# Optimization experiments

Hardware: AMD Instinct MI355X
Metric: run time of the kernel (lower is better)

The kernel has to match this reference:

```python
import jax, jax.numpy as jnp
import numpy as np
from jax import lax

EPS = 1e-6
DN = ('NCHW', 'OIHW', 'NCHW')


def cconv2d(x, wr, wi, br, bi, padding, dilation, groups):
    """Complex conv2d: x [B,2,C,H,W]; (a+ib)*(c+id) convolution with per-part bias.
    real = conv(xr,wr)+br - (conv(xi,wi)+bi); imag = conv(xi,wr)+br + conv(xr,wi)+bi."""
    B = x.shape[0]
    x2 = jnp.concatenate([x[:, 0], x[:, 1]], axis=0)  # [2B,C,H,W] stack re/im in batch
    pad = [(padding[0], padding[0]), (padding[1], padding[1])]

    def conv(w):
        return lax.conv_general_dilated(x2, w, (1, 1), pad, rhs_dilation=dilation,
                                        dimension_numbers=DN, feature_group_count=groups)

    cr = conv(wr)
    ci = conv(wi)
    real = cr[:B] - ci[B:] + (br - bi)[None, :, None, None]
    imag = cr[B:] + ci[:B] + (br + bi)[None, :, None, None]
    return jnp.stack([real, imag], axis=1)


def parallel_conv1d(t, wr, wi, br, bi, ch_out, kernel, dilation=1):
    """Grouped per-frequency complex conv. t: [B,2,Cin,N,T] -> [B,2,ch_out,N,T] (causal)."""
    B, _, Cin, N, T = t.shape
    pad = kernel * dilation - dilation
    x = jnp.transpose(t, (0, 1, 3, 2, 4))  # [B,2,N,Cin,T]; channels=N, groups=N
    y = cconv2d(x, wr, wi, br, bi, (0, pad), (1, dilation), N)  # [B,2,N*ch_out,1,T+pad]
    y = y[..., pad:]  # trim -> causal, length T
    y = y.reshape(B, 2, N, ch_out, T)
    return jnp.transpose(y, (0, 1, 3, 2, 4))


def cAct(t):
    return jnp.stack([jnp.tanh(t[:, 0]), jax.nn.relu(t[:, 1])], axis=1)


def cLog(t):
    re, im = t[:, 0], t[:, 1]
    mag = jnp.sqrt(re * re + im * im)
    return jnp.stack([jnp.log(mag + EPS), jnp.arctan2(im, re)], axis=1)


def cExp(t):
    mag = jnp.exp(t[:, 0])
    return jnp.stack([mag * jnp.cos(t[:, 1]), mag * jnp.sin(t[:, 1])], axis=1)


FREQS, CH_IN, CH_INNER, FREQ_K, TIME_K, DIL = 256, 8, 32, 3, 5, 2


def setup_inputs() -> dict:
    key = jax.random.key(0)
    ks = jax.random.split(key, 17)
    s = 0.05
    d = {'tensor': jax.random.normal(ks[0], (4, 2, CH_IN, FREQS, 1000), jnp.float32)}
    # channel_shuffle: ParallelConv1d(freqs, ch_in, ch_inner, 1) -> weight [N*ch_inner,1,ch_in,1]
    d['cs_wr'] = jax.random.normal(ks[1], (FREQS * CH_INNER, 1, CH_IN, 1), jnp.float32) * s
    d['cs_wi'] = jax.random.normal(ks[2], (FREQS * CH_INNER, 1, CH_IN, 1), jnp.float32) * s
    d['cs_br'] = jax.random.normal(ks[3], (FREQS * CH_INNER,), jnp.float32) * s
    d['cs_bi'] = jax.random.normal(ks[4], (FREQS * CH_INNER,), jnp.float32) * s
    # freq_conv: depthwise ComplexConv2d(ch_inner, ch_inner, (freq_kernel,1), groups=ch_inner)
    d['fc_wr'] = jax.random.normal(ks[5], (CH_INNER, 1, FREQ_K, 1), jnp.float32) * s
    d['fc_wi'] = jax.random.normal(ks[6], (CH_INNER, 1, FREQ_K, 1), jnp.float32) * s
    d['fc_br'] = jax.random.normal(ks[7], (CH_INNER,), jnp.float32) * s
    d['fc_bi'] = jax.random.normal(ks[8], (CH_INNER,), jnp.float32) * s
    # time_conv: ParallelConv1d(freqs, ch_inner, ch_in, time_kernel, dilation)
    d['tc_wr'] = jax.random.normal(ks[9], (FREQS * CH_IN, 1, CH_INNER, TIME_K), jnp.float32) * s
    d['tc_wi'] = jax.random.normal(ks[10], (FREQS * CH_IN, 1, CH_INNER, TIME_K), jnp.float32) * s
    d['tc_br'] = jax.random.normal(ks[11], (FREQS * CH_IN,), jnp.float32) * s
    d['tc_bi'] = jax.random.normal(ks[12], (FREQS * CH_IN,), jnp.float32) * s
    # last: ParallelConv1d(freqs, ch_in, ch_in, 1)
    d['last_wr'] = jax.random.normal(ks[13], (FREQS * CH_IN, 1, CH_IN, 1), jnp.float32) * s
    d['last_wi'] = jax.random.normal(ks[14], (FREQS * CH_IN, 1, CH_IN, 1), jnp.float32) * s
    d['last_br'] = jax.random.normal(ks[15], (FREQS * CH_IN,), jnp.float32) * s
    d['last_bi'] = jax.random.normal(ks[16], (FREQS * CH_IN,), jnp.float32) * s
    return d


def reference(tensor, cs_wr, cs_wi, cs_br, cs_bi, fc_wr, fc_wi, fc_br, fc_bi,
              tc_wr, tc_wi, tc_br, tc_bi, last_wr, last_wi, last_br, last_bi):
    t = cLog(tensor)                                                    # [B,2,Cin,N,T]
    t = parallel_conv1d(t, cs_wr, cs_wi, cs_br, cs_bi, CH_INNER, 1)     # [B,2,Cinner,N,T]
    t = cAct(t)
    t = cconv2d(t, fc_wr, fc_wi, fc_br, fc_bi, (FREQ_K // 2, 0), (1, 1), CH_INNER)
    t = cAct(t)
    t = parallel_conv1d(t, tc_wr, tc_wi, tc_br, tc_bi, CH_IN, TIME_K, DIL)
    t = cAct(t)
    t = cExp(t)
    t = parallel_conv1d(t, last_wr, last_wi, last_br, last_bi, CH_IN, 1)
    return t
```

## Files before the change

### kernel.cpp

```cpp
#include <hip/hip_runtime.h>
#include <math.h>

#define TLEN 1000
#define NF 256
#define CIN 8
#define CMID 32
#define TK 5
#define TT 120
#define THA 128
#define T2R 136
#define SLS 72

#define CSW_OFF  0u
#define CB_OFF   1048576u
#define FCP_OFF  1114112u
#define FCB_OFF  1114880u
#define TCW_OFF  1115136u
#define TCB_OFF  3736576u
#define LA_OFF   3752960u
#define LAB_OFF  4015104u
#define XLOG_OFF 4031488u
#define WS_NEED  36799488u

typedef _Float16 f16x8 __attribute__((ext_vector_type(8)));
typedef _Float16 f16x4 __attribute__((ext_vector_type(4)));
typedef _Float16 f16x2 __attribute__((ext_vector_type(2)));
typedef float f32x4 __attribute__((ext_vector_type(4)));

__device__ __forceinline__ float ftanh(float x) {
    float e = __expf(2.0f * x);
    return 1.0f - 2.0f / (e + 1.0f);
}

__device__ __forceinline__ float fatan2(float y, float x) {
    float ax = fabsf(x), ay = fabsf(y);
    float mx = fmaxf(fmaxf(ax, ay), 1e-30f);
    float mn = fminf(ax, ay);
    float a = mn * __builtin_amdgcn_rcpf(mx);
    float s = a * a;
    float r = fmaf(s, fmaf(s, fmaf(s, fmaf(s, fmaf(s, -0.0117212f, 0.05265332f),
                -0.11643287f), 0.19354346f), -0.33262347f), 0.99997726f);
    r *= a;
    if (ay > ax) r = 1.5707964f - r;
    if (x < 0.0f) r = 3.1415927f - r;
    return copysignf(r, y);
}

__global__ __launch_bounds__(256) void mb_pack(
    const float* __restrict__ cswr, const float* __restrict__ cswi,
    const float* __restrict__ csbr, const float* __restrict__ csbi,
    const float* __restrict__ fcwr, const float* __restrict__ fcwi,
    const float* __restrict__ fcbr, const float* __restrict__ fcbi,
    const float* __restrict__ tcwr, const float* __restrict__ tcwi,
    const float* __restrict__ tcbr, const float* __restrict__ tcbi,
    const float* __restrict__ lawr, const float* __restrict__ lawi,
    const float* __restrict__ labr, const float* __restrict__ labi,
    unsigned char* __restrict__ ws)
{
    int e = blockIdx.x * 256 + threadIdx.x;
    if (e < 32768) {
        int fp = e >> 7, ca = (e >> 2) & 31, g = e & 3;
        f16x8 aRe = (f16x8){0,0,0,0,0,0,0,0}, aIm = (f16x8){0,0,0,0,0,0,0,0};
        if (g < 2) {
            const float* wr = cswr + ((size_t)fp*CMID + ca)*CIN + g*4;
            const float* wi = cswi + ((size_t)fp*CMID + ca)*CIN + g*4;
#pragma unroll
            for (int r = 0; r < 4; ++r) {
                float a = wr[r], bb = wi[r];
                aRe[2*r] = (_Float16)a;  aRe[2*r+1] = (_Float16)(-bb);
                aIm[2*r] = (_Float16)bb; aIm[2*r+1] = (_Float16)a;
            }
        }
        *(f16x8*)(ws + CSW_OFF + (size_t)e*32)      = aRe;
        *(f16x8*)(ws + CSW_OFF + (size_t)e*32 + 16) = aIm;
        return;
    }
    e -= 32768;
    if (e < 8192) {
        int fp = e >> 5, c = e & 31;
        float br = csbr[fp*CMID + c], bi = csbi[fp*CMID + c];
        *(float2*)(ws + CB_OFF + (size_t)e*8) = make_float2(br - bi, br + bi);
        return;
    }
    e -= 8192;
    if (e < 96) {
        int j = e / 32, c = e % 32;
        *(float2*)(ws + FCP_OFF + (size_t)e*8) = make_float2(fcwr[c*3 + j], fcwi[c*3 + j]);
        return;
    }
    e -= 96;
    if (e < 32) {
        *(float2*)(ws + FCB_OFF + (size_t)e*8) = make_float2(fcbr[e] - fcbi[e], fcbr[e] + fcbi[e]);
        return;
    }
    e -= 32;
    if (e < 163840) {
        int idx = e % 640;
        int f   = e / 640;
        int m   = idx / 40;
        int r2  = idx % 40;
        int g   = r2 / 10;
        int i10 = r2 % 10;
        int kt = i10 >> 1, kc = i10 & 1;
        int co = m & 7;
        f16x8 v;
#pragma unroll
        for (int j = 0; j < 8; ++j) {
            int ci = kc*16 + g*4 + (j >> 1);
            int p  = j & 1;
            float a  = tcwr[(((size_t)f*CIN + co)*CMID + ci)*TK + kt];
            float bb = tcwi[(((size_t)f*CIN + co)*CMID + ci)*TK + kt];
            float val = (m < 8) ? (p ? -bb : a) : (p ? a : bb);
            v[j] = (_Float16)val;
        }
        *(f16x8*)(ws + TCW_OFF + (size_t)e*16) = v;
        return;
    }
    e -= 163840;
    if (e < 4096) {
        int f = e >> 4, m = e & 15, co = m & 7;
        float br = tcbr[f*CIN + co], bi = tcbi[f*CIN + co];
        *(float*)(ws + TCB_OFF + (size_t)e*4) = (m >= 8) ? (br + bi) : (br - bi);
        return;
    }
    e -= 4096;
    if (e < 16384) {
        int f = e >> 6, m = (e >> 2) & 15, g = e & 3, co = m & 7;
        f16x8 v = (f16x8){0,0,0,0,0,0,0,0};
        if (g < 2) {
#pragma unroll
            for (int j = 0; j < 8; ++j) {
                int ci = g*4 + (j >> 1);
                int p  = j & 1;
                float a  = lawr[((size_t)f*CIN + co)*CIN + ci];
                float bb = lawi[((size_t)f*CIN + co)*CIN + ci];
                float val = (m < 8) ? (p ? -bb : a) : (p ? a : bb);
                v[j] = (_Float16)val;
            }
        }
        *(f16x8*)(ws + LA_OFF + (size_t)e*16) = v;
        return;
    }
    e -= 16384;
    if (e < 4096) {
        int f = e >> 4, m = e & 15, co = m & 7;
        float br = labr[f*CIN + co], bi = labi[f*CIN + co];
        *(float*)(ws + LAB_OFF + (size_t)e*4) = (m >= 8) ? (br + bi) : (br - bi);
    }
}

__global__ __launch_bounds__(256) void mb_xlog(
    const float* __restrict__ x, unsigned char* __restrict__ ws)
{
    const int tid = threadIdx.x;
    const int chunk = blockIdx.x;
    const int f = blockIdx.y;
    const int b = blockIdx.z;
    const int t00 = chunk * 128;

    __shared__ __align__(16) _Float16 sl[128 * 16];

    const float* xr_base = x + ((size_t)(b*2+0)*CIN)*NF*TLEN + (size_t)f*TLEN;
    const float* xi_base = x + ((size_t)(b*2+1)*CIN)*NF*TLEN + (size_t)f*TLEN;
#pragma unroll
    for (int it = 0; it < 4; ++it) {
        int i  = it*256 + tid;
        int tl = i & 127, ci = i >> 7;
        int tg = t00 + tl;
        float lr = 0.f, li = 0.f;
        if (tg < TLEN) {
            float vr = xr_base[(size_t)ci*NF*TLEN + tg];
            float vi = xi_base[(size_t)ci*NF*TLEN + tg];
            lr = __logf(sqrtf(fmaf(vr, vr, vi*vi)) + 1e-6f);
            li = fatan2(vi, vr);
        }
        *(f16x2*)&sl[tl*16 + ci*2] = (f16x2){(_Float16)lr, (_Float16)li};
    }
    __syncthreads();
    if (tid < 128) {
        int tg = t00 + tid;
        if (tg < TLEN) {
            unsigned char* dst = ws + XLOG_OFF + ((size_t)(b*NF + f)*1000 + tg)*32;
            *(f16x8*)dst        = *(const f16x8*)&sl[tid*16];
            *(f16x8*)(dst + 16) = *(const f16x8*)&sl[tid*16 + 8];
        }
    }
}

__device__ __forceinline__ int t2r_off(int tl, int kc, int g) {
    int byte = tl * 128 + kc * 64 + g * 16;
    byte ^= (tl & 7) << 4;
    return byte;
}

__global__ __launch_bounds__(256, 4) void mb_main(
    const unsigned char* __restrict__ ws, float* __restrict__ out)
{
    const int tid  = threadIdx.x;
    const int tb   = blockIdx.x;
    const int f    = blockIdx.y;
    const int b    = blockIdx.z;
    const int t0   = tb * TT;
    const int lane = tid & 63;
    const int w    = tid >> 6;
    const int col  = lane & 15;
    const int g    = lane >> 4;

    __shared__ __align__(16) unsigned char s_t2h[T2R * 128];
    __shared__ __align__(16) float s_y[THA][17];
    _Float16* s_e = (_Float16*)s_t2h;

    ((unsigned int*)s_t2h)[THA*32 + tid] = 0u;

    const f16x8*  cswp = (const f16x8*)(ws + CSW_OFF);
    const float4* cb4  = (const float4*)(ws + CB_OFF);
    const f16x8*  tcp  = (const f16x8*)(ws + TCW_OFF);
    const float4* tb4  = (const float4*)(ws + TCB_OFF);
    const f16x8*  lap  = (const f16x8*)(ws + LA_OFF);
    const float4* lb4  = (const float4*)(ws + LAB_OFF);

    const int cBase  = (w & 1) * 16;
    const int ntBase = (w >> 1) * 4;
    const int ca = cBase + col;
    const int cg = cBase + 4*g;

    int toff[4];
    {
        int tbv = t0 + ntBase*16 + col;
#pragma unroll
        for (int q = 0; q < 4; ++q) {
            int t = tbv + q*16; if (t > 999) t = 999;
            toff[q] = t*32 + (g & 1)*16;
        }
    }
    const int awoff = (ca*4 + g)*2;
    const int cboff = cg >> 1;

    f32x4 accR[4], accI[4];
#pragma unroll
    for (int q = 0; q < 4; ++q) { accR[q] = (f32x4){0,0,0,0}; accI[q] = (f32x4){0,0,0,0}; }

#define STAGE_A_J(J)                                                          \
    { const int fp = f - 1 + (J);                                             \
      if (fp >= 0 && fp < NF) {                                               \
        f16x8 aRe = cswp[fp*256 + awoff];                                     \
        f16x8 aIm = cswp[fp*256 + awoff + 1];                                 \
        float4 c01 = cb4[fp*16 + cboff], c23 = cb4[fp*16 + cboff + 1];        \
        float4 fc01 = *(const float4*)(ws + FCP_OFF + ((J)*32 + cg)*8);       \
        float4 fc23 = *(const float4*)(ws + FCP_OFF + ((J)*32 + cg)*8 + 16);  \
        const unsigned char* xb = ws + XLOG_OFF + (size_t)(b*NF + fp)*32000;  \
        float bm[4] = {c01.x, c01.z, c23.x, c23.z};                           \
        float bp[4] = {c01.y, c01.w, c23.y, c23.w};                           \
        float fr[4] = {fc01.x, fc01.z, fc23.x, fc23.z};                       \
        float fi[4] = {fc01.y, fc01.w, fc23.y, fc23.w};                       \
        _Pragma("unroll")                                                     \
        for (int q = 0; q < 4; ++q) {                                         \
            f16x8 bf = *(const f16x8*)(xb + toff[q]);                         \
            f32x4 dRe = __builtin_amdgcn_mfma_f32_16x16x32_f16(aRe, bf, (f32x4){0,0,0,0}, 0, 0, 0); \
            f32x4 dIm = __builtin_amdgcn_mfma_f32_16x16x32_f16(aIm, bf, (f32x4){0,0,0,0}, 0, 0, 0); \
            _Pragma("unroll")                                                 \
            for (int r = 0; r < 4; ++r) {                                     \
                float ar = ftanh(dRe[r] + bm[r]);                             \
                float ai = fmaxf(dIm[r] + bp[r], 0.f);                        \
                accR[q][r] = fmaf(fr[r], ar, fmaf(-fi[r], ai, accR[q][r]));   \
                accI[q][r] = fmaf(fr[r], ai, fmaf( fi[r], ar, accI[q][r]));   \
            }                                                                 \
        } } }

    STAGE_A_J(0)
    STAGE_A_J(1)
    STAGE_A_J(2)
#undef STAGE_A_J

    {
        float4 fb01 = *(const float4*)(ws + FCB_OFF + cg*8);
        float4 fb23 = *(const float4*)(ws + FCB_OFF + cg*8 + 16);
        float fbm[4] = {fb01.x, fb01.z, fb23.x, fb23.z};
        float fbp[4] = {fb01.y, fb01.w, fb23.y, fb23.w};
#pragma unroll
        for (int q = 0; q < 4; ++q) {
            int tp = ntBase*16 + q*16 + col;
            bool pad = (t0 + tp >= TLEN);
            f16x8 v;
#pragma unroll
            for (int r = 0; r < 4; ++r) {
                float tr = ftanh(accR[q][r] + fbm[r]);
                float ti = fmaxf(accI[q][r] + fbp[r], 0.f);
                v[2*r]   = (_Float16)tr;
                v[2*r+1] = (_Float16)ti;
            }
            if (pad) v = (f16x8){0,0,0,0,0,0,0,0};
            int addr = (tp*128 + cg*4) ^ ((tp & 7) << 4);
            *(f16x8*)&s_t2h[addr] = v;
        }
    }

    f16x8 afr[10];
    {
        int base = ((f*16 + col)*4 + g)*10;
#pragma unroll
        for (int kk = 0; kk < 10; ++kk) afr[kk] = tcp[base + kk];
    }
    __syncthreads();

    {
        const int tb0 = w * 32, tb1 = tb0 + 16;
        f32x4 acc0 = {0,0,0,0}, acc1 = {0,0,0,0};
#pragma unroll
        for (int kt = 0; kt < 5; ++kt) {
#pragma unroll
            for (int kc = 0; kc < 2; ++kc) {
                f16x8 b0 = *(const f16x8*)&s_t2h[t2r_off(tb0 + col + 2*kt, kc, g)];
                f16x8 b1 = *(const f16x8*)&s_t2h[t2r_off(tb1 + col + 2*kt, kc, g)];
                acc0 = __builtin_amdgcn_mfma_f32_16x16x32_f16(afr[kt*2+kc], b0, acc0, 0, 0, 0);
                acc1 = __builtin_amdgcn_mfma_f32_16x16x32_f16(afr[kt*2+kc], b1, acc1, 0, 0, 0);
            }
        }
        float4 tcb = tb4[f*4 + g];
        float tcbv[4] = {tcb.x, tcb.y, tcb.z, tcb.w};
#pragma unroll
        for (int r = 0; r < 4; ++r) {
            int mm = g*4 + r;
            s_y[tb0 + col][mm] = acc0[r] + tcbv[r];
            s_y[tb1 + col][mm] = acc1[r] + tcbv[r];
        }
    }
    __syncthreads();

#pragma unroll
    for (int it = 0; it < 4; ++it) {
        int i  = it*256 + tid;
        int co = i >> 7, tl = i & 127;
        float yR = s_y[tl][co];
        float yI = s_y[tl][co + 8];
        float mg = __expf(ftanh(yR));
        float ph = fmaxf(yI, 0.f);
        float sn, cs;
        __sincosf(ph, &sn, &cs);
        *(f16x2*)&s_e[tl*16 + co*2] = (f16x2){(_Float16)(mg * cs), (_Float16)(mg * sn)};
    }
    __syncthreads();

    {
        f16x8 dA = lap[(f*16 + col)*4 + g];
        float4 lb = lb4[f*4 + g];
        float lbv[4] = {lb.x, lb.y, lb.z, lb.w};
        float* obase = out + (size_t)b*4096000 + (size_t)f*TLEN + t0;
        int ooff[4];
#pragma unroll
        for (int r = 0; r < 4; ++r) {
            int m = g*4 + r;
            ooff[r] = (m >> 3)*2048000 + (m & 7)*256000;
        }
#pragma unroll
        for (int t2 = 0; t2 < 2; ++t2) {
            int tp = (w*2 + t2)*16 + col;
            f16x8 eB = (g < 2) ? *(const f16x8*)&s_e[tp*16 + g*8]
                               : (f16x8){0,0,0,0,0,0,0,0};
            f32x4 o = __builtin_amdgcn_mfma_f32_16x16x32_f16(dA, eB, (f32x4){0,0,0,0}, 0, 0, 0);
            if (tp < TT && t0 + tp < TLEN) {
#pragma unroll
                for (int r = 0; r < 4; ++r)
                    obase[ooff[r] + tp] = o[r] + lbv[r];
            }
        }
    }
}

__device__ __forceinline__ int t2_off_fb(int tl, int p, int c) {
    int byte = tl * 128 + p * 64 + c * 2;
    byte ^= (tl & 7) << 4;
    return byte >> 1;
}

__global__ __launch_bounds__(256, 4) void mb_fused_fb(
    const float* __restrict__ x,
    const float* __restrict__ cswr, const float* __restrict__ cswi,
    const float* __restrict__ csbr, const float* __restrict__ csbi,
    const float* __restrict__ fcwr, const float* __restrict__ fcwi,
    const float* __restrict__ fcbr, const float* __restrict__ fcbi,
    const float* __restrict__ tcwr, const float* __restrict__ tcwi,
    const float* __restrict__ tcbr, const float* __restrict__ tcbi,
    const float* __restrict__ lawr, const float* __restrict__ lawi,
    const float* __restrict__ labr, const float* __restrict__ labi,
    float* __restrict__ out)
{
    const int tid  = threadIdx.x;
    const int tb   = blockIdx.x;
    const int f    = blockIdx.y;
    const int b    = blockIdx.z;
    const int t0   = tb * TT;
    const int lane = tid & 63;
    const int w    = tid >> 6;
    const int col  = lane & 15;
    const int g    = lane >> 4;

    __shared__ __align__(16) _Float16 s_t2h[T2R * 2 * CMID];
    __shared__ __align__(16) unsigned char s_u[THA * SLS];
    float (*s_y)[17] = (float (*)[17])s_u;

    for (int r = tid; r < THA; r += 256) {
        unsigned int* p = (unsigned int*)(s_u + r * SLS + 32);
        p[0] = 0x00003C00u;
#pragma unroll
        for (int q = 1; q < 8; ++q) p[q] = 0u;
    }
    ((unsigned int*)s_t2h)[THA*32 + tid] = 0u;

    const int cBase  = (w & 1) * 16;
    const int ntBase = (w >> 1) * 4;
    f32x4 accR[4], accI[4];
#pragma unroll
    for (int q = 0; q < 4; ++q) { accR[q] = (f32x4){0,0,0,0}; accI[q] = (f32x4){0,0,0,0}; }

    for (int j = 0; j < 3; ++j) {
        const int fp = f - 1 + j;
        if (fp < 0 || fp >= NF) continue;
        __syncthreads();
        const float* xr_base = x + ((size_t)(b*2+0)*CIN)*NF*TLEN + (size_t)fp*TLEN;
        const float* xi_base = x + ((size_t)(b*2+1)*CIN)*NF*TLEN + (size_t)fp*TLEN;
#pragma unroll
        for (int it = 0; it < 4; ++it) {
            int i  = it*256 + tid;
            int tl = i & 127, ci = i >> 7;
            int tg = t0 + tl;
            float lr = 0.f, li = 0.f;
            if (tg < TLEN) {
                float vr = xr_base[(size_t)ci*NF*TLEN + tg];
                float vi = xi_base[(size_t)ci*NF*TLEN + tg];
                lr = __logf(sqrtf(fmaf(vr, vr, vi*vi)) + 1e-6f);
                li = fatan2(vi, vr);
            }
            *(f16x2*)(s_u + tl*SLS + ci*4) = (f16x2){(_Float16)lr, (_Float16)li};
        }
        __syncthreads();
        const int ca = cBase + col;
        const float4 wrv = *(const float4*)(cswr + ((size_t)fp*CMID + ca)*CIN + (g & 1)*4);
        const float4 wiv = *(const float4*)(cswi + ((size_t)fp*CMID + ca)*CIN + (g & 1)*4);
        const float bR = csbr[fp*CMID + ca], bI = csbi[fp*CMID + ca];
        f16x8 aRe, aIm;
        if (g < 2) {
            aRe = (f16x8){(_Float16)wrv.x, (_Float16)(-wiv.x), (_Float16)wrv.y, (_Float16)(-wiv.y),
                          (_Float16)wrv.z, (_Float16)(-wiv.z), (_Float16)wrv.w, (_Float16)(-wiv.w)};
            aIm = (f16x8){(_Float16)wiv.x, (_Float16)wrv.x, (_Float16)wiv.y, (_Float16)wrv.y,
                          (_Float16)wiv.z, (_Float16)wrv.z, (_Float16)wiv.w, (_Float16)wrv.w};
        } else if (g == 2) {
            aRe = (f16x8){(_Float16)(bR - bI), 0, 0, 0, 0, 0, 0, 0};
            aIm = (f16x8){(_Float16)(bR + bI), 0, 0, 0, 0, 0, 0, 0};
        } else {
            aRe = (f16x8){0,0,0,0,0,0,0,0};
            aIm = (f16x8){0,0,0,0,0,0,0,0};
        }
        float frj[4], fij[4];
#pragma unroll
        for (int r = 0; r < 4; ++r) {
            int c = cBase + g*4 + r;
            frj[r] = fcwr[c*3 + j];
            fij[r] = fcwi[c*3 + j];
        }
#pragma unroll
        for (int q = 0; q < 4; ++q) {
            int tp = (ntBase + q)*16 + col;
            const unsigned char* bp = s_u + tp*SLS + g*16;
            f16x4 blo = *(const f16x4*)bp;
            f16x4 bhi = *(const f16x4*)(bp + 8);
            f16x8 bf = __builtin_shufflevector(blo, bhi, 0, 1, 2, 3, 4, 5, 6, 7);
            f32x4 dRe = __builtin_amdgcn_mfma_f32_16x16x32_f16(aRe, bf, (f32x4){0,0,0,0}, 0, 0, 0);
            f32x4 dIm = __builtin_amdgcn_mfma_f32_16x16x32_f16(aIm, bf, (f32x4){0,0,0,0}, 0, 0, 0);
#pragma unroll
            for (int r = 0; r < 4; ++r) {
                float ar = ftanh(dRe[r]);
                float ai = fmaxf(dIm[r], 0.f);
                accR[q][r] = fmaf(frj[r], ar, fmaf(-fij[r], ai, accR[q][r]));
                accI[q][r] = fmaf(frj[r], ai, fmaf( fij[r], ar, accI[q][r]));
            }
        }
    }
    {
        float fbr[4], fbi[4];
#pragma unroll
        for (int r = 0; r < 4; ++r) {
            int c = cBase + g*4 + r;
            fbr[r] = fcbr[c]; fbi[r] = fcbi[c];
        }
#pragma unroll
        for (int q = 0; q < 4; ++q) {
            int tp = (ntBase + q)*16 + col;
            bool pad = (t0 + tp >= TLEN);
#pragma unroll
            for (int r = 0; r < 4; ++r) {
                int c = cBase + g*4 + r;
                float tr = ftanh(accR[q][r] + (fbr[r] - fbi[r]));
                float ti = fmaxf(accI[q][r] + (fbr[r] + fbi[r]), 0.f);
                if (pad) { tr = 0.f; ti = 0.f; }
                s_t2h[t2_off_fb(tp, 0, c)] = (_Float16)tr;
                s_t2h[t2_off_fb(tp, 1, c)] = (_Float16)ti;
            }
        }
    }
    f16x8 afr[10];
    {
        const bool isI = col >= 8;
        const int co = col & 7;
        const float* wrp = tcwr + (size_t)(f*CIN + co)*(CMID*TK) + g*(8*TK);
        const float* wip = tcwi + (size_t)(f*CIN + co)*(CMID*TK) + g*(8*TK);
#pragma unroll
        for (int q = 0; q < 10; ++q) {
            float4 a4 = *(const float4*)&wrp[q*4];
            float4 b4 = *(const float4*)&wip[q*4];
#pragma unroll
            for (int r = 0; r < 4; ++r) {
                const int idx = q*4 + r;
                const int jj  = idx / 5;
                const int kt  = idx % 5;
                float a  = (r==0)?a4.x:(r==1)?a4.y:(r==2)?a4.z:a4.w;
                float bv = (r==0)?b4.x:(r==1)?b4.y:(r==2)?b4.z:b4.w;
                afr[kt][jj]      = (_Float16)(isI ? bv : a);
                afr[kt + TK][jj] = (_Float16)(isI ? a : -bv);
            }
        }
    }
    __syncthreads();
    {
        const int tb0 = w * 32, tb1 = tb0 + 16;
        f32x4 acc0 = {0,0,0,0}, acc1 = {0,0,0,0};
#pragma unroll
        for (int kk = 0; kk < 10; ++kk) {
            int p  = (kk < 5) ? 0 : 1;
            int kt = (kk < 5) ? kk : kk - 5;
            f16x8 b0 = *(const f16x8*)&s_t2h[t2_off_fb(tb0 + col + 2*kt, p, g*8)];
            f16x8 b1 = *(const f16x8*)&s_t2h[t2_off_fb(tb1 + col + 2*kt, p, g*8)];
            acc0 = __builtin_amdgcn_mfma_f32_16x16x32_f16(afr[kk], b0, acc0, 0, 0, 0);
            acc1 = __builtin_amdgcn_mfma_f32_16x16x32_f16(afr[kk], b1, acc1, 0, 0, 0);
        }
#pragma unroll
        for (int r = 0; r < 4; ++r) {
            int mm = g*4 + r;
            int coo = mm & 7;
            float bRv = tcbr[f*CIN + coo], bIv = tcbi[f*CIN + coo];
            float bias = (mm >= 8) ? (bRv + bIv) : (bRv - bIv);
            s_y[tb0 + col][mm] = acc0[r] + bias;
            s_y[tb1 + col][mm] = acc1[r] + bias;
        }
    }
    __syncthreads();
#pragma unroll
    for (int it = 0; it < 4; ++it) {
        int i  = it*256 + tid;
        int co = i >> 7, tl = i & 127;
        float yR = s_y[tl][co];
        float yI = s_y[tl][co + 8];
        float mg = __expf(ftanh(yR));
        float ph = fmaxf(yI, 0.f);
        float sn, cs;
        __sincosf(ph, &sn, &cs);
        s_y[tl][co]     = mg * cs;
        s_y[tl][co + 8] = mg * sn;
    }
    __syncthreads();
#pragma unroll
    for (int it = 0; it < 4; ++it) {
        int i   = it*256 + tid;
        int tl2 = i & 127;
        int co2 = __builtin_amdgcn_readfirstlane(i >> 7);
        int tg  = t0 + tl2;
        if (tl2 < TT && tg < TLEN) {
            const float4* lr4 = (const float4*)(lawr + ((size_t)f*CIN + co2)*CIN);
            const float4* li4 = (const float4*)(lawi + ((size_t)f*CIN + co2)*CIN);
            float4 a0 = lr4[0], a1 = lr4[1];
            float4 b0 = li4[0], b1 = li4[1];
            float oR = 0.f, oI = 0.f;
#pragma unroll
            for (int co = 0; co < CIN; ++co) {
                float er = s_y[tl2][co];
                float ei = s_y[tl2][co + 8];
                float a  = (co < 4) ? ((co==0)?a0.x:(co==1)?a0.y:(co==2)?a0.z:a0.w)
                                    : ((co==4)?a1.x:(co==5)?a1.y:(co==6)?a1.z:a1.w);
                float bb = (co < 4) ? ((co==0)?b0.x:(co==1)?b0.y:(co==2)?b0.z:b0.w)
                                    : ((co==4)?b1.x:(co==5)?b1.y:(co==6)?b1.z:b1.w);
                oR = fmaf(a, er, fmaf(-bb, ei, oR));
                oI = fmaf(a, ei, fmaf( bb, er, oI));
            }
            float br = labr[f*CIN + co2], bi = labi[f*CIN + co2];
            oR += br - bi;
            oI += br + bi;
            out[((size_t)(b*2+0)*CIN + co2)*NF*TLEN + (size_t)f*TLEN + tg] = oR;
            out[((size_t)(b*2+1)*CIN + co2)*NF*TLEN + (size_t)f*TLEN + tg] = oI;
        }
    }
}

extern "C" void kernel_launch(void* const* d_in, const int* in_sizes, int n_in,
                              void* d_out, int out_size, void* d_ws, size_t ws_size,
                              hipStream_t stream) {
    const float* p[17];
    for (int i = 0; i < 17; ++i) p[i] = (const float*)d_in[i];

    if (ws_size >= WS_NEED) {
        unsigned char* ws = (unsigned char*)d_ws;
        mb_pack<<<dim3(897), 256, 0, stream>>>(
            p[1], p[2], p[3], p[4],
            p[5], p[6], p[7], p[8],
            p[9], p[10], p[11], p[12],
            p[13], p[14], p[15], p[16], ws);
        mb_xlog<<<dim3(8, NF, 4), 256, 0, stream>>>(p[0], ws);
        mb_main<<<dim3(9, NF, 4), 256, 0, stream>>>(ws, (float*)d_out);
    } else {
        mb_fused_fb<<<dim3(9, NF, 4), 256, 0, stream>>>(
            p[0],
            p[1], p[2], p[3], p[4],
            p[5], p[6], p[7], p[8],
            p[9], p[10], p[11], p[12],
            p[13], p[14], p[15], p[16],
            (float*)d_out);
    }
}
```

Baseline: 165.6 us.

## Precompute channel-shuffle stage once per frequency instead of three times in main kernel

```diff
diff --git a/kernel.cpp b/kernel.cpp
--- a/kernel.cpp
+++ b/kernel.cpp
@@ -19,8 +19,10 @@
 #define TCB_OFF  3736576u
 #define LA_OFF   3752960u
 #define LAB_OFF  4015104u
-#define XLOG_OFF 4031488u
-#define WS_NEED  36799488u
+#define T1_OFF   4031488u
+#define T1_BATCH 32768000u
+#define WS_ONE   36799488u
+#define WS_ALL   135103488u
 
 typedef _Float16 f16x8 __attribute__((ext_vector_type(8)));
 typedef _Float16 f16x4 __attribute__((ext_vector_type(4)));
@@ -149,14 +151,19 @@
     }
 }
 
-__global__ __launch_bounds__(256) void mb_xlog(
-    const float* __restrict__ x, unsigned char* __restrict__ ws)
+__global__ __launch_bounds__(256, 6) void mb_t1(
+    const float* __restrict__ x, unsigned char* __restrict__ ws,
+    int b0, unsigned int t1zstride)
 {
-    const int tid = threadIdx.x;
+    const int tid   = threadIdx.x;
     const int chunk = blockIdx.x;
-    const int f = blockIdx.y;
-    const int b = blockIdx.z;
-    const int t00 = chunk * 128;
+    const int f     = blockIdx.y;
+    const int b     = b0 + blockIdx.z;
+    const int t00   = chunk * 128;
+    const int lane  = tid & 63;
+    const int w     = tid >> 6;
+    const int col   = lane & 15;
+    const int g     = lane >> 4;
 
     __shared__ __align__(16) _Float16 sl[128 * 16];
 
@@ -177,13 +184,36 @@
         *(f16x2*)&sl[tl*16 + ci*2] = (f16x2){(_Float16)lr, (_Float16)li};
     }
     __syncthreads();
-    if (tid < 128) {
-        int tg = t00 + tid;
-        if (tg < TLEN) {
-            unsigned char* dst = ws + XLOG_OFF + ((size_t)(b*NF + f)*1000 + tg)*32;
-            *(f16x8*)dst        = *(const f16x8*)&sl[tid*16];
-            *(f16x8*)(dst + 16) = *(const f16x8*)&sl[tid*16 + 8];
-        }
+
+    const f16x8*  cswp = (const f16x8*)(ws + CSW_OFF);
+    const float4* cb4  = (const float4*)(ws + CB_OFF);
+    const int cBase  = (w & 1) * 16;
+    const int ntBase = (w >> 1) * 4;
+    const int ca = cBase + col;
+    const int cg = cBase + 4*g;
+    int abase = (f*128 + ca*4 + g)*2;
+    f16x8 aRe = cswp[abase], aIm = cswp[abase + 1];
+    int cb0 = f*16 + (cg >> 1);
+    float4 c01 = cb4[cb0], c23 = cb4[cb0 + 1];
+    float bm[4] = {c01.x, c01.z, c23.x, c23.z};
+    float bp[4] = {c01.y, c01.w, c23.y, c23.w};
+    unsigned char* t1base = ws + T1_OFF + (size_t)blockIdx.z * t1zstride
+                            + (size_t)f * 128000u;
+#pragma unroll
+    for (int q = 0; q < 4; ++q) {
+        int tn = (ntBase + q)*16 + col;
+        f16x8 bf = *(const f16x8*)&sl[tn*16 + (g & 1)*8];
+        f32x4 dRe = __builtin_amdgcn_mfma_f32_16x16x32_f16(aRe, bf, (f32x4){0,0,0,0}, 0, 0, 0);
+        f32x4 dIm = __builtin_amdgcn_mfma_f32_16x16x32_f16(aIm, bf, (f32x4){0,0,0,0}, 0, 0, 0);
+        f16x8 v;
+#pragma unroll
+        for (int r = 0; r < 4; ++r) {
+            v[2*r]   = (_Float16)ftanh(dRe[r] + bm[r]);
+            v[2*r+1] = (_Float16)fmaxf(dIm[r] + bp[r], 0.f);
+        }
+        int tg = t00 + tn;
+        if (tg < TLEN)
+            *(f16x8*)(t1base + (size_t)tg*128u + cg*4) = v;
     }
 }
 
@@ -194,12 +224,14 @@
 }
 
 __global__ __launch_bounds__(256, 4) void mb_main(
-    const unsigned char* __restrict__ ws, float* __restrict__ out)
+    const unsigned char* __restrict__ ws, float* __restrict__ out,
+    int b0, unsigned int t1zstride)
 {
     const int tid  = threadIdx.x;
-    const int tb   = blockIdx.x;
-    const int f    = blockIdx.y;
-    const int b    = blockIdx.z;
+    const int d    = blockIdx.x;
+    const int f    = (d & 7)*32 + ((d >> 3) & 31);
+    const int tb   = d >> 8;
+    const int b    = b0 + blockIdx.z;
     const int t0   = tb * TT;
     const int lane = tid & 63;
     const int w    = tid >> 6;
@@ -212,16 +244,14 @@
 
     ((unsigned int*)s_t2h)[THA*32 + tid] = 0u;
 
-    const f16x8*  cswp = (const f16x8*)(ws + CSW_OFF);
-    const float4* cb4  = (const float4*)(ws + CB_OFF);
     const f16x8*  tcp  = (const f16x8*)(ws + TCW_OFF);
     const float4* tb4  = (const float4*)(ws + TCB_OFF);
     const f16x8*  lap  = (const f16x8*)(ws + LA_OFF);
     const float4* lb4  = (const float4*)(ws + LAB_OFF);
+    const unsigned char* t1base = ws + T1_OFF + (size_t)blockIdx.z * t1zstride;
 
     const int cBase  = (w & 1) * 16;
     const int ntBase = (w >> 1) * 4;
-    const int ca = cBase + col;
     const int cg = cBase + 4*g;
 
     int toff[4];
@@ -230,47 +260,38 @@
 #pragma unroll
         for (int q = 0; q < 4; ++q) {
             int t = tbv + q*16; if (t > 999) t = 999;
-            toff[q] = t*32 + (g & 1)*16;
-        }
-    }
-    const int awoff = (ca*4 + g)*2;
-    const int cboff = cg >> 1;
+            toff[q] = t*128 + cg*4;
+        }
+    }
 
     f32x4 accR[4], accI[4];
 #pragma unroll
     for (int q = 0; q < 4; ++q) { accR[q] = (f32x4){0,0,0,0}; accI[q] = (f32x4){0,0,0,0}; }
 
-#define STAGE_A_J(J)                                                          \
+#define FC_J(J)                                                               \
     { const int fp = f - 1 + (J);                                             \
       if (fp >= 0 && fp < NF) {                                               \
-        f16x8 aRe = cswp[fp*256 + awoff];                                     \
-        f16x8 aIm = cswp[fp*256 + awoff + 1];                                 \
-        float4 c01 = cb4[fp*16 + cboff], c23 = cb4[fp*16 + cboff + 1];        \
+        const unsigned char* xb = t1base + (size_t)fp * 128000u;              \
         float4 fc01 = *(const float4*)(ws + FCP_OFF + ((J)*32 + cg)*8);       \
         float4 fc23 = *(const float4*)(ws + FCP_OFF + ((J)*32 + cg)*8 + 16);  \
-        const unsigned char* xb = ws + XLOG_OFF + (size_t)(b*NF + fp)*32000;  \
-        float bm[4] = {c01.x, c01.z, c23.x, c23.z};                           \
-        float bp[4] = {c01.y, c01.w, c23.y, c23.w};                           \
         float fr[4] = {fc01.x, fc01.z, fc23.x, fc23.z};                       \
         float fi[4] = {fc01.y, fc01.w, fc23.y, fc23.w};                       \
         _Pragma("unroll")                                                     \
         for (int q = 0; q < 4; ++q) {                                         \
-            f16x8 bf = *(const f16x8*)(xb + toff[q]);                         \
-            f32x4 dRe = __builtin_amdgcn_mfma_f32_16x16x32_f16(aRe, bf, (f32x4){0,0,0,0}, 0, 0, 0); \
-            f32x4 dIm = __builtin_amdgcn_mfma_f32_16x16x32_f16(aIm, bf, (f32x4){0,0,0,0}, 0, 0, 0); \
+            f16x8 hv = *(const f16x8*)(xb + toff[q]);                         \
             _Pragma("unroll")                                                 \
             for (int r = 0; r < 4; ++r) {                                     \
-                float ar = ftanh(dRe[r] + bm[r]);                             \
-                float ai = fmaxf(dIm[r] + bp[r], 0.f);                        \
+                float ar = (float)hv[2*r];                                    \
+                float ai = (float)hv[2*r+1];                                  \
                 accR[q][r] = fmaf(fr[r], ar, fmaf(-fi[r], ai, accR[q][r]));   \
                 accI[q][r] = fmaf(fr[r], ai, fmaf( fi[r], ar, accI[q][r]));   \
             }                                                                 \
         } } }
 
-    STAGE_A_J(0)
-    STAGE_A_J(1)
-    STAGE_A_J(2)
-#undef STAGE_A_J
+    FC_J(0)
+    FC_J(1)
+    FC_J(2)
+#undef FC_J
 
     {
         float4 fb01 = *(const float4*)(ws + FCB_OFF + cg*8);
@@ -596,15 +617,22 @@
     const float* p[17];
     for (int i = 0; i < 17; ++i) p[i] = (const float*)d_in[i];
 
-    if (ws_size >= WS_NEED) {
+    if (ws_size >= WS_ONE) {
         unsigned char* ws = (unsigned char*)d_ws;
         mb_pack<<<dim3(897), 256, 0, stream>>>(
             p[1], p[2], p[3], p[4],
             p[5], p[6], p[7], p[8],
             p[9], p[10], p[11], p[12],
             p[13], p[14], p[15], p[16], ws);
-        mb_xlog<<<dim3(8, NF, 4), 256, 0, stream>>>(p[0], ws);
-        mb_main<<<dim3(9, NF, 4), 256, 0, stream>>>(ws, (float*)d_out);
+        if (ws_size >= WS_ALL) {
+            mb_t1<<<dim3(8, NF, 4), 256, 0, stream>>>(p[0], ws, 0, T1_BATCH);
+            mb_main<<<dim3(2304, 1, 4), 256, 0, stream>>>(ws, (float*)d_out, 0, T1_BATCH);
+        } else {
+            for (int b = 0; b < 4; ++b) {
+                mb_t1<<<dim3(8, NF, 1), 256, 0, stream>>>(p[0], ws, b, 0u);
+                mb_main<<<dim3(2304, 1, 1), 256, 0, stream>>>(ws, (float*)d_out, b, 0u);
+            }
+        }
     } else {
         mb_fused_fb<<<dim3(9, NF, 4), 256, 0, stream>>>(
             p[0],
```

After: 168.0 us. No clear change (+1.5%).
